# Optimization experiments

Measured on AMD Instinct MI355X. Metric: run time of the kernel, lower is better.

Reference implementation:

```python
import jax, jax.numpy as jnp
import numpy as np

EMB_DIM = 1024
N_HEAD = 16
HEAD_DIM = EMB_DIM // N_HEAD


def setup_inputs() -> dict:
    key = jax.random.key(0)
    kx, kq, kk, kv, ko = jax.random.split(key, 5)
    B, S = 4, 2048
    x = jax.random.normal(kx, (B, S, EMB_DIM), dtype=jnp.float32)
    attention_mask = jnp.ones((B, S), dtype=jnp.int32)
    s = 1.0 / np.sqrt(EMB_DIM)
    w_q = jax.random.normal(kq, (EMB_DIM, EMB_DIM), dtype=jnp.float32) * s
    w_k = jax.random.normal(kk, (EMB_DIM, EMB_DIM), dtype=jnp.float32) * s
    w_v = jax.random.normal(kv, (EMB_DIM, EMB_DIM), dtype=jnp.float32) * s
    w_o = jax.random.normal(ko, (EMB_DIM, EMB_DIM), dtype=jnp.float32) * s
    return {"x": x, "attention_mask": attention_mask,
            "w_q": w_q, "w_k": w_k, "w_v": w_v, "w_o": w_o}


def reference(x, attention_mask, w_q, w_k, w_v, w_o):
    B, S, _ = x.shape
    scale = 1.0 / np.sqrt(HEAD_DIM)
    # projections; nn.Linear computes x @ W^T
    def split_heads(t):
        return t.reshape(B, S, N_HEAD, HEAD_DIM).transpose(0, 2, 1, 3)  # [B,H,S,D]
    q = split_heads(x @ w_q.T)
    k = split_heads(x @ w_k.T)
    v = split_heads(x @ w_v.T)
    scores = jnp.einsum('bhqd,bhkd->bhqk', q, k) * scale  # [B,H,S,S]
    pad_mask = (attention_mask == 0)[:, None, None, :]          # [B,1,1,S]
    causal = jnp.triu(jnp.ones((S, S), dtype=bool), k=1)[None, None]  # [1,1,S,S]
    combined = pad_mask | causal
    scores = jnp.where(combined, -jnp.inf, scores)
    attn = jax.nn.softmax(scores, axis=-1)
    out = jnp.einsum('bhqk,bhkd->bhqd', attn, v)
    out = out.transpose(0, 2, 1, 3).reshape(B, S, EMB_DIM)
    return out @ w_o.T
```

## Files before the change

kernel.cpp:

```cpp
#include <hip/hip_runtime.h>

typedef __bf16 bf16x8 __attribute__((ext_vector_type(8)));
typedef float f32x4 __attribute__((ext_vector_type(4)));

#define LOG2E 1.4426950408889634f
#define NEGC (-12.0f * LOG2E)

__device__ inline unsigned short f2bf(float f) {
  unsigned int u = __builtin_bit_cast(unsigned int, f);
  u += 0x7fff + ((u >> 16) & 1);
  return (unsigned short)(u >> 16);
}

__device__ inline void async16(const void* g, void* l) {
  __builtin_amdgcn_global_load_lds(
      (__attribute__((address_space(1))) void*)(g),
      (__attribute__((address_space(3))) void*)(l), 16, 0, 0);
}

__global__ __launch_bounds__(256) void cast_all(
    const float* __restrict__ x, const float* __restrict__ w0,
    const float* __restrict__ w1, const float* __restrict__ w2,
    const float* __restrict__ w3, unsigned short* __restrict__ xb,
    unsigned short* __restrict__ ob ) {
  int id = blockIdx.x;
  const float* in;
  unsigned short* out;
  int boff;
  if (id < 8192) { in = x; out = xb; boff = id; }
  else {
    int w = (id - 8192) >> 10; boff = (id - 8192) & 1023;
    switch (w) { case 0: in = w0; break; case 1: in = w1; break;
                 case 2: in = w2; break; default: in = w3; }
    out = ob + (long)w * 1048576;
  }
  int i = (boff * 256 + threadIdx.x) * 4;
  float4 v = *(const float4*)(in + i);
  ushort4 o;
  o.x = f2bf(v.x); o.y = f2bf(v.y); o.z = f2bf(v.z); o.w = f2bf(v.w);
  *(ushort4*)(out + i) = o;
}

#define BM 128
#define BN 128
#define BK 32

__global__ __launch_bounds__(256, 3) void gemm_bt(
    const unsigned short* __restrict__ A, const unsigned short* __restrict__ W,
    void* __restrict__ out, int M, int N, int K, int mode) {
  __shared__ unsigned short SM[BM * BK + BN * BK];
  unsigned short* As = SM;
  unsigned short* Ws = SM + BM * BK;
  int tid = threadIdx.x;
  int lane = tid & 63, wid = tid >> 6;
  int wm = wid >> 1, wn = wid & 1;
  int l15 = lane & 15, quad = lane >> 4;
  int m0 = (blockIdx.x & 63) * BM, n0 = (blockIdx.x >> 6) * BN;

  f32x4 acc[4][4] = {};

  int srow = tid >> 2;
  int scol = (tid & 3) * 8;
  const unsigned short* Ag = A + (long)(m0 + srow) * K + scol;
  const unsigned short* Wg = W + (long)(n0 + srow) * K + scol;
  char* AsB = (char*)As + wid * 1024;
  char* WsB = (char*)Ws + wid * 1024;

  for (int kt = 0; kt < K; kt += BK) {
    __syncthreads();
    async16(Ag + kt, AsB);
    async16(Ag + kt + (long)64 * K, AsB + 4096);
    async16(Wg + kt, WsB);
    async16(Wg + kt + (long)64 * K, WsB + 4096);
    __syncthreads();
    bf16x8 af[4], wf[4];
#pragma unroll
    for (int t = 0; t < 4; t++)
      af[t] = *(const bf16x8*)(As + (wm * 64 + t * 16 + l15) * BK + quad * 8);
#pragma unroll
    for (int t = 0; t < 4; t++)
      wf[t] = *(const bf16x8*)(Ws + (wn * 64 + t * 16 + l15) * BK + quad * 8);
#pragma unroll
    for (int i = 0; i < 4; i++)
#pragma unroll
      for (int j = 0; j < 4; j++)
        acc[i][j] = __builtin_amdgcn_mfma_f32_16x16x32_bf16(af[i], wf[j], acc[i][j], 0, 0, 0);
  }

  if (mode == 0) {
    float* Cf = (float*)out;
#pragma unroll
    for (int i = 0; i < 4; i++) {
      int row = m0 + wm * 64 + i * 16 + quad * 4;
#pragma unroll
      for (int j = 0; j < 4; j++) {
        int col = n0 + wn * 64 + j * 16 + l15;
#pragma unroll
        for (int r = 0; r < 4; r++)
          Cf[(long)(row + r) * N + col] = acc[i][j][r];
      }
    }
  } else {
    unsigned short* Cb = (unsigned short*)out;
    int which = n0 >> 10;
    if (which == 2) {
#pragma unroll
      for (int i = 0; i < 4; i++)
#pragma unroll
        for (int j = 0; j < 4; j++) {
          int m = m0 + wm * 64 + i * 16 + quad * 4;
          int n = n0 + wn * 64 + j * 16 + l15;
          int nn = n & 1023;
          int b = m >> 11, s = m & 2047;
          int h = nn >> 6, d = nn & 63;
          ushort4 pk;
          pk.x = f2bf(acc[i][j][0]); pk.y = f2bf(acc[i][j][1]);
          pk.z = f2bf(acc[i][j][2]); pk.w = f2bf(acc[i][j][3]);
          *(ushort4*)(&Cb[16777216 + (((long)((b * 16 + h) * 64 + d)) << 11) + s]) = pk;
        }
    } else {
      float scale = (which == 0) ? 0.125f : 1.0f;
      int h0 = (n0 & 1023) >> 6;
      unsigned short* Es = SM;
#pragma unroll
      for (int qr = 0; qr < 4; qr++) {
        __syncthreads();
        if (wm == (qr >> 1)) {
#pragma unroll
          for (int ii = 0; ii < 2; ii++) {
            int i = (qr & 1) * 2 + ii;
#pragma unroll
            for (int j = 0; j < 4; j++)
#pragma unroll
              for (int r = 0; r < 4; r++) {
                int rr = (i & 1) * 16 + quad * 4 + r;
                Es[rr * 136 + wn * 64 + j * 16 + l15] = f2bf(acc[i][j][r] * scale);
              }
          }
        }
        __syncthreads();
#pragma unroll
        for (int p = 0; p < 2; p++) {
          int pair = p * 32 + (tid >> 3);
          int rq = pair >> 1;
          int head = pair & 1, c8 = tid & 7;
          uint4 v = *(const uint4*)(&Es[rq * 136 + head * 64 + c8 * 8]);
          int m = m0 + qr * 32 + rq;
          int b = m >> 11, s = m & 2047;
          int h = h0 + head;
          long idx = (long)which * 8388608 +
                     ((long)((b * 16 + h) * 2048 + s)) * 64 + c8 * 8;
          *(uint4*)(&Cb[idx]) = v;
        }
      }
    }
  }
}

__global__ __launch_bounds__(512, 2)
void gemm256(
    const unsigned short* __restrict__ A, const unsigned short* __restrict__ W,
    unsigned short* __restrict__ out, int M, int N, int K) {
  __shared__ unsigned short sm[65536];
  (void)N;
  int tid = threadIdx.x, lane = tid & 63, wid = tid >> 6;
  int wm = wid >> 2, wn = wid & 3;
  int l15 = lane & 15, quad = lane >> 4;

  int cpx = (int)gridDim.x >> 3;
  int id = (int)blockIdx.x;
  int swz = (id & 7) * cpx + (id >> 3);
  int mtiles = M >> 8;
  int mt = swz % mtiles, nt = swz / mtiles;
  int m0 = mt << 8, n0 = nt << 8;

  f32x4 acc[8][4] = {};
  bf16x8 afr[4][2], bfr[2][2];

  int rl = tid >> 3;
  int ch = (tid & 7) ^ (rl & 7);
  const unsigned short* Ag = A + (long)(m0 + rl) * K + ch * 8;
  const unsigned short* Wg = W + (long)(n0 + rl) * K + ch * 8;
  int dst0 = wid * 1024;

#define STG(BUF, MAT, HALF, KT) do {                                          \
    const unsigned short* g_ = ((MAT) ? Wg : Ag) + (long)(HALF) * 128 * K + (KT) * 64; \
    char* d_ = (char*)sm + ((BUF) * 4 + (MAT) * 2 + (HALF)) * 16384 + dst0;   \
    async16(g_, d_);                                                          \
    async16(g_ + (long)64 * K, d_ + 8192);                                    \
  } while (0)

#define RDA(BUF, MH) do {                                                     \
    char* b_ = (char*)sm + ((BUF) * 4 + (MH)) * 16384;                        \
    _Pragma("unroll") for (int mf = 0; mf < 4; mf++) {                        \
      int r_ = wm * 64 + mf * 16 + l15;                                       \
      char* p_ = b_ + r_ * 128; int sw_ = (r_ & 7) << 4;                      \
      afr[mf][0] = *(const bf16x8*)(p_ + ((quad * 16) ^ sw_));                \
      afr[mf][1] = *(const bf16x8*)(p_ + ((64 + quad * 16) ^ sw_));           \
    } } while (0)

#define RDB(BUF, NH) do {                                                     \
    char* b_ = (char*)sm + ((BUF) * 4 + 2 + (NH)) * 16384;                    \
    _Pragma("unroll") for (int nf = 0; nf < 2; nf++) {                        \
      int r_ = wn * 32 + nf * 16 + l15;                                       \
      char* p_ = b_ + r_ * 128; int sw_ = (r_ & 7) << 4;                      \
      bfr[nf][0] = *(const bf16x8*)(p_ + ((quad * 16) ^ sw_));                \
      bfr[nf][1] = *(const bf16x8*)(p_ + ((64 + quad * 16) ^ sw_));           \
    } } while (0)

#define MM16(MH, NH) do {                                                     \
    __builtin_amdgcn_s_setprio(1);                                            \
    _Pragma("unroll") for (int kk = 0; kk < 2; kk++)                          \
    _Pragma("unroll") for (int mf = 0; mf < 4; mf++)                          \
    _Pragma("unroll") for (int nf = 0; nf < 2; nf++)                          \
      acc[(MH) * 4 + mf][(NH) * 2 + nf] = __builtin_amdgcn_mfma_f32_16x16x32_bf16( \
          afr[mf][kk], bfr[nf][kk], acc[(MH) * 4 + mf][(NH) * 2 + nf], 0, 0, 0);   \
    __builtin_amdgcn_s_setprio(0);                                            \
  } while (0)

#define BARx() __builtin_amdgcn_s_barrier()
#define LGKM0() asm volatile("s_waitcnt lgkmcnt(0)" ::: "memory")
#define VM8() asm volatile("s_waitcnt vmcnt(8)" ::: "memory")
#define VM0() asm volatile("s_waitcnt vmcnt(0)" ::: "memory")

  STG(0, 0, 0, 0); STG(0, 1, 0, 0); STG(0, 1, 1, 0); STG(0, 0, 1, 0);
  STG(1, 0, 0, 1); STG(1, 1, 0, 1);
  asm volatile("s_waitcnt vmcnt(4)" ::: "memory");
  BARx();

  for (int i = 0; i < 8; i++) {
    int t1 = 2 * i + 1;
    bool st = (i < 7);
    RDA(0, 0); RDB(0, 0); STG(1, 1, 1, t1);
    BARx(); LGKM0(); MM16(0, 0); VM8(); BARx();
    RDB(0, 1); STG(1, 0, 1, t1);
    BARx(); LGKM0(); MM16(0, 1); VM8(); BARx();
    RDA(0, 1); RDB(0, 0); if (st) STG(0, 0, 0, t1 + 1);
    BARx(); LGKM0(); MM16(1, 0); VM8(); BARx();
    RDB(0, 1); if (st) STG(0, 1, 0, t1 + 1);
    BARx(); LGKM0(); MM16(1, 1); if (st) VM8(); else VM0(); BARx();
    RDA(1, 0); RDB(1, 0); if (st) STG(0, 1, 1, t1 + 1);
    BARx(); LGKM0(); MM16(0, 0); if (st) VM8(); else VM0(); BARx();
    RDB(1, 1); if (st) STG(0, 0, 1, t1 + 1);
    BARx(); LGKM0(); MM16(0, 1); if (st) VM8(); else VM0(); BARx();
    RDA(1, 1); RDB(1, 0); if (st) STG(1, 0, 0, t1 + 2);
    BARx(); LGKM0(); MM16(1, 0); if (st) VM8(); else VM0(); BARx();
    RDB(1, 1); if (st) STG(1, 1, 0, t1 + 2);
    BARx(); LGKM0(); MM16(1, 1); if (st) VM8(); else VM0(); BARx();
  }

#undef STG
#undef RDA
#undef RDB
#undef MM16
#undef BARx
#undef LGKM0
#undef VM8
#undef VM0

  unsigned short* Cb = out;
  int which = n0 >> 10;
  if (which == 2) {
#pragma unroll
    for (int mi = 0; mi < 8; mi++) {
      int m = m0 + (mi >> 2) * 128 + wm * 64 + (mi & 3) * 16 + quad * 4;
      int b = m >> 11, s = m & 2047;
#pragma unroll
      for (int ni = 0; ni < 4; ni++) {
        int n = n0 + (ni >> 1) * 128 + wn * 32 + (ni & 1) * 16 + l15;
        int nn = n & 1023;
        int h = nn >> 6, d = nn & 63;
        ushort4 pk;
        pk.x = f2bf(acc[mi][ni][0]); pk.y = f2bf(acc[mi][ni][1]);
        pk.z = f2bf(acc[mi][ni][2]); pk.w = f2bf(acc[mi][ni][3]);
        *(ushort4*)(&Cb[16777216 + (((long)((b * 16 + h) * 64 + d)) << 11) + s]) = pk;
      }
    }
  } else {
    float scale = (which == 0) ? 0.125f : 1.0f;
#pragma unroll
    for (int mi = 0; mi < 8; mi++) {
#pragma unroll
      for (int ni = 0; ni < 4; ni++) {
#pragma unroll
        for (int r = 0; r < 4; r++) {
          int m = m0 + (mi >> 2) * 128 + wm * 64 + (mi & 3) * 16 + quad * 4 + r;
          int n = n0 + (ni >> 1) * 128 + wn * 32 + (ni & 1) * 16 + l15;
          int b = m >> 11, s = m & 2047;
          int nn = n & 1023;
          int h = nn >> 6, d = nn & 63;
          long idx = (long)which * 8388608 + ((long)((b * 16 + h) * 2048 + s)) * 64 + d;
          Cb[idx] = f2bf(acc[mi][ni][r] * scale);
        }
      }
    }
  }
}

#define BQ 128
#define BKV 64
#define PSTR 76

__global__ __launch_bounds__(256, 3) void attn(
    const unsigned short* __restrict__ Q, const unsigned short* __restrict__ Kt,
    const unsigned short* __restrict__ VT, const int* __restrict__ am,
    unsigned short* __restrict__ O) {
  __shared__ unsigned short QPs[BQ * PSTR];
  __shared__ unsigned short Ks[BKV * PSTR];
  __shared__ unsigned short Vs[64 * PSTR];
  const int S = 2048, D = 64;
  int tid = threadIdx.x, lane = tid & 63, wid = tid >> 6;
  int l15 = lane & 15, quad = lane >> 4;

  int id = blockIdx.x;
  int s = id >> 8;
  int r = id & 255;
  int bh = r & 63;
  int c = r >> 6;
  int qt;
  switch (s) { case 0: qt = 15 - c; break; case 1: qt = 8 + c; break;
               case 2: qt = 7 - c; break; default: qt = c; }
  int q0 = qt * BQ;
  int b = bh >> 4, h = bh & 15;
  const unsigned short* Qg = Q + (long)bh * S * D;
  const unsigned short* Kg = Kt + (long)bh * S * D;
  const unsigned short* Vg = VT + (long)bh * D * S;
  const int* amg = am + b * S;

  int row0 = tid >> 3, col0 = (tid & 7) * 8;
  int row1 = 32 + (tid >> 3), col1 = col0;

#pragma unroll
  for (int rr = 0; rr < 4; rr++) {
    int cc = rr * 256 + tid;
    int row = cc >> 3, col = (cc & 7) * 8;
    *(uint4*)(&QPs[row * PSTR + col]) = *(const uint4*)(Qg + (long)(q0 + row) * D + col);
  }

  uint4 kreg0 = *(const uint4*)(Kg + (long)row0 * D + col0);
  uint4 kreg1 = *(const uint4*)(Kg + (long)row1 * D + col1);
  uint4 vreg0 = *(const uint4*)(Vg + (long)row0 * S + col0);
  uint4 vreg1 = *(const uint4*)(Vg + (long)row1 * S + col1);

  __syncthreads();
  bf16x8 qf[2][2];
#pragma unroll
  for (int i = 0; i < 2; i++)
#pragma unroll
    for (int kk = 0; kk < 2; kk++)
      qf[i][kk] = *(const bf16x8*)(&QPs[(wid * 32 + i * 16 + l15) * PSTR + kk * 32 + quad * 8]);

  f32x4 o_acc[2][4] = {};
  float lsum[2][4] = {};

  int tFull = q0 >> 6;
  int nt = tFull + 2;
  for (int t = 0; t < nt; t++) {
    int s0 = t * BKV;
    __syncthreads();
    *(uint4*)(&Ks[row0 * PSTR + col0]) = kreg0;
    *(uint4*)(&Ks[row1 * PSTR + col1]) = kreg1;
    *(uint4*)(&Vs[row0 * PSTR + col0]) = vreg0;
    *(uint4*)(&Vs[row1 * PSTR + col1]) = vreg1;
    __syncthreads();

    {
      long s0n = (t + 1) * BKV; if (s0n > S - BKV) s0n = S - BKV;
      kreg0 = *(const uint4*)(Kg + (s0n + row0) * D + col0);
      kreg1 = *(const uint4*)(Kg + (s0n + row1) * D + col1);
      vreg0 = *(const uint4*)(Vg + (long)row0 * S + s0n + col0);
      vreg1 = *(const uint4*)(Vg + (long)row1 * S + s0n + col1);
    }

    int mvj[4];
#pragma unroll
    for (int j = 0; j < 4; j++) mvj[j] = amg[s0 + j * 16 + l15];

    f32x4 sacc[2][4] = {};
#pragma unroll
    for (int kk = 0; kk < 2; kk++) {
      bf16x8 kf[4];
#pragma unroll
      for (int j = 0; j < 4; j++)
        kf[j] = *(const bf16x8*)(&Ks[(j * 16 + l15) * PSTR + kk * 32 + quad * 8]);
      __builtin_amdgcn_s_setprio(1);
#pragma unroll
      for (int i = 0; i < 2; i++)
#pragma unroll
        for (int j = 0; j < 4; j++)
          sacc[i][j] = __builtin_amdgcn_mfma_f32_16x16x32_bf16(qf[i][kk], kf[j], sacc[i][j], 0, 0, 0);
      __builtin_amdgcn_s_setprio(0);
    }

    float fb[4];
#pragma unroll
    for (int j = 0; j < 4; j++) fb[j] = mvj[j] ? NEGC : -1e38f;

    if (t < tFull) {
#pragma unroll
      for (int i = 0; i < 2; i++)
#pragma unroll
        for (int rr = 0; rr < 4; rr++) {
          int prow = (wid * 32 + i * 16 + quad * 4 + rr) * PSTR;
          float rs = 0.f;
#pragma unroll
          for (int j = 0; j < 4; j++) {
            float p = __builtin_amdgcn_exp2f(fmaf(sacc[i][j][rr], LOG2E, fb[j]));
            unsigned int u = __builtin_bit_cast(unsigned int, p);
            QPs[prow + j * 16 + l15] = (unsigned short)(u >> 16);
            rs += __builtin_bit_cast(float, u & 0xffff0000u);
          }
          lsum[i][rr] += rs;
        }
    } else {
#pragma unroll
      for (int i = 0; i < 2; i++)
#pragma unroll
        for (int rr = 0; rr < 4; rr++) {
          int row = q0 + wid * 32 + i * 16 + quad * 4 + rr;
          int prow = (wid * 32 + i * 16 + quad * 4 + rr) * PSTR;
          float rs = 0.f;
#pragma unroll
          for (int j = 0; j < 4; j++) {
            int col = s0 + j * 16 + l15;
            float fbe = (col > row) ? -1e38f : fb[j];
            float p = __builtin_amdgcn_exp2f(fmaf(sacc[i][j][rr], LOG2E, fbe));
            unsigned int u = __builtin_bit_cast(unsigned int, p);
            QPs[prow + j * 16 + l15] = (unsigned short)(u >> 16);
            rs += __builtin_bit_cast(float, u & 0xffff0000u);
          }
          lsum[i][rr] += rs;
        }
    }

#pragma unroll
    for (int kk = 0; kk < 2; kk++) {
      bf16x8 pf[2], vf[4];
#pragma unroll
      for (int i = 0; i < 2; i++)
        pf[i] = *(const bf16x8*)(&QPs[(wid * 32 + i * 16 + l15) * PSTR + kk * 32 + quad * 8]);
#pragma unroll
      for (int j = 0; j < 4; j++)
        vf[j] = *(const bf16x8*)(&Vs[(j * 16 + l15) * PSTR + kk * 32 + quad * 8]);
      __builtin_amdgcn_s_setprio(1);
#pragma unroll
      for (int i = 0; i < 2; i++)
#pragma unroll
        for (int j = 0; j < 4; j++)
          o_acc[i][j] = __builtin_amdgcn_mfma_f32_16x16x32_bf16(pf[i], vf[j], o_acc[i][j], 0, 0, 0);
      __builtin_amdgcn_s_setprio(0);
    }
  }

#pragma unroll
  for (int i = 0; i < 2; i++)
#pragma unroll
    for (int rr = 0; rr < 4; rr++) {
      float tsum = lsum[i][rr];
      tsum += __shfl_xor(tsum, 1, 64);
      tsum += __shfl_xor(tsum, 2, 64);
      tsum += __shfl_xor(tsum, 4, 64);
      tsum += __shfl_xor(tsum, 8, 64);
      float inv = 1.0f / tsum;
      int prow = (wid * 32 + i * 16 + quad * 4 + rr) * PSTR;
#pragma unroll
      for (int j = 0; j < 4; j++)
        QPs[prow + j * 16 + l15] = f2bf(o_acc[i][j][rr] * inv);
    }
  __syncthreads();
#pragma unroll
  for (int rr = 0; rr < 4; rr++) {
    int cc = rr * 256 + tid;
    int row = cc >> 3, col = (cc & 7) * 8;
    uint4 v = *(const uint4*)(&QPs[row * PSTR + col]);
    long gm = (long)b * S + q0 + row;
    *(uint4*)(&O[gm * 1024 + h * 64 + col]) = v;
  }
}

extern "C" void kernel_launch(void* const* d_in, const int* in_sizes, int n_in,
                              void* d_out, int out_size, void* d_ws, size_t ws_size,
                              hipStream_t stream) {
  const float* x  = (const float*)d_in[0];
  const int*   am = (const int*)d_in[1];
  const float* wq = (const float*)d_in[2];
  const float* wk = (const float*)d_in[3];
  const float* wv = (const float*)d_in[4];
  const float* wo = (const float*)d_in[5];
  float* out = (float*)d_out;

  const int S = 2048, E = 1024, Bb = 4, H = 16;
  const int M = Bb * S;

  char* ws = (char*)d_ws;
  unsigned short* xb  = (unsigned short*)ws;
  unsigned short* wqb = (unsigned short*)(ws + 16777216);
  unsigned short* wob = wqb + 3 * 1048576;
  unsigned short* Qb  = (unsigned short*)(ws + 25165824);
  unsigned short* Ob  = Qb + 25165824;

  cast_all<<<12288, 256, 0, stream>>>(x, wq, wk, wv, wo, xb, wqb);

  gemm_bt<<<dim3((3 * E / BN) * (M / BM)), 256, 0, stream>>>(xb, wqb, Qb, M, 3 * E, E, 4);
  attn<<<dim3(1024), 256, 0, stream>>>(Qb, Qb + 8388608, Qb + 16777216, am, Ob);
  gemm_bt<<<dim3((E / BN) * (M / BM)), 256, 0, stream>>>(Ob, wob, out, M, E, E, 0);
}
```

Measured before the change: 249.1 us.

## Double-buffer K tiles in LDS and stream V fragments from global to registers

Restructures the attention loop so K tiles are double-buffered in shared memory. This needs one barrier per iteration instead of two, and the next-next K tile is prefetched into registers. V no longer goes through shared memory: each wave loads its MFMA V fragments straight from global memory into registers one tile ahead. The aim is to cut barrier stalls and LDS round trips, at the cost of redundant V reads across waves through the cache and more registers. The unused gemm256 kernel is also deleted.

Result: slower. 307.8 us (+23.5%).

```diff
diff --git a/kernel.cpp b/kernel.cpp
--- a/kernel.cpp
+++ b/kernel.cpp
@@ -157,146 +157,6 @@
   }
 }
 
-__global__ __launch_bounds__(512, 2)
-void gemm256(
-    const unsigned short* __restrict__ A, const unsigned short* __restrict__ W,
-    unsigned short* __restrict__ out, int M, int N, int K) {
-  __shared__ unsigned short sm[65536];
-  (void)N;
-  int tid = threadIdx.x, lane = tid & 63, wid = tid >> 6;
-  int wm = wid >> 2, wn = wid & 3;
-  int l15 = lane & 15, quad = lane >> 4;
-
-  int cpx = (int)gridDim.x >> 3;
-  int id = (int)blockIdx.x;
-  int swz = (id & 7) * cpx + (id >> 3);
-  int mtiles = M >> 8;
-  int mt = swz % mtiles, nt = swz / mtiles;
-  int m0 = mt << 8, n0 = nt << 8;
-
-  f32x4 acc[8][4] = {};
-  bf16x8 afr[4][2], bfr[2][2];
-
-  int rl = tid >> 3;
-  int ch = (tid & 7) ^ (rl & 7);
-  const unsigned short* Ag = A + (long)(m0 + rl) * K + ch * 8;
-  const unsigned short* Wg = W + (long)(n0 + rl) * K + ch * 8;
-  int dst0 = wid * 1024;
-
-#define STG(BUF, MAT, HALF, KT) do {                                          \
-    const unsigned short* g_ = ((MAT) ? Wg : Ag) + (long)(HALF) * 128 * K + (KT) * 64; \
-    char* d_ = (char*)sm + ((BUF) * 4 + (MAT) * 2 + (HALF)) * 16384 + dst0;   \
-    async16(g_, d_);                                                          \
-    async16(g_ + (long)64 * K, d_ + 8192);                                    \
-  } while (0)
-
-#define RDA(BUF, MH) do {                                                     \
-    char* b_ = (char*)sm + ((BUF) * 4 + (MH)) * 16384;                        \
-    _Pragma("unroll") for (int mf = 0; mf < 4; mf++) {                        \
-      int r_ = wm * 64 + mf * 16 + l15;                                       \
-      char* p_ = b_ + r_ * 128; int sw_ = (r_ & 7) << 4;                      \
-      afr[mf][0] = *(const bf16x8*)(p_ + ((quad * 16) ^ sw_));                \
-      afr[mf][1] = *(const bf16x8*)(p_ + ((64 + quad * 16) ^ sw_));           \
-    } } while (0)
-
-#define RDB(BUF, NH) do {                                                     \
-    char* b_ = (char*)sm + ((BUF) * 4 + 2 + (NH)) * 16384;                    \
-    _Pragma("unroll") for (int nf = 0; nf < 2; nf++) {                        \
-      int r_ = wn * 32 + nf * 16 + l15;                                       \
-      char* p_ = b_ + r_ * 128; int sw_ = (r_ & 7) << 4;                      \
-      bfr[nf][0] = *(const bf16x8*)(p_ + ((quad * 16) ^ sw_));                \
-      bfr[nf][1] = *(const bf16x8*)(p_ + ((64 + quad * 16) ^ sw_));           \
-    } } while (0)
-
-#define MM16(MH, NH) do {                                                     \
-    __builtin_amdgcn_s_setprio(1);                                            \
-    _Pragma("unroll") for (int kk = 0; kk < 2; kk++)                          \
-    _Pragma("unroll") for (int mf = 0; mf < 4; mf++)                          \
-    _Pragma("unroll") for (int nf = 0; nf < 2; nf++)                          \
-      acc[(MH) * 4 + mf][(NH) * 2 + nf] = __builtin_amdgcn_mfma_f32_16x16x32_bf16( \
-          afr[mf][kk], bfr[nf][kk], acc[(MH) * 4 + mf][(NH) * 2 + nf], 0, 0, 0);   \
-    __builtin_amdgcn_s_setprio(0);                                            \
-  } while (0)
-
-#define BARx() __builtin_amdgcn_s_barrier()
-#define LGKM0() asm volatile("s_waitcnt lgkmcnt(0)" ::: "memory")
-#define VM8() asm volatile("s_waitcnt vmcnt(8)" ::: "memory")
-#define VM0() asm volatile("s_waitcnt vmcnt(0)" ::: "memory")
-
-  STG(0, 0, 0, 0); STG(0, 1, 0, 0); STG(0, 1, 1, 0); STG(0, 0, 1, 0);
-  STG(1, 0, 0, 1); STG(1, 1, 0, 1);
-  asm volatile("s_waitcnt vmcnt(4)" ::: "memory");
-  BARx();
-
-  for (int i = 0; i < 8; i++) {
-    int t1 = 2 * i + 1;
-    bool st = (i < 7);
-    RDA(0, 0); RDB(0, 0); STG(1, 1, 1, t1);
-    BARx(); LGKM0(); MM16(0, 0); VM8(); BARx();
-    RDB(0, 1); STG(1, 0, 1, t1);
-    BARx(); LGKM0(); MM16(0, 1); VM8(); BARx();
-    RDA(0, 1); RDB(0, 0); if (st) STG(0, 0, 0, t1 + 1);
-    BARx(); LGKM0(); MM16(1, 0); VM8(); BARx();
-    RDB(0, 1); if (st) STG(0, 1, 0, t1 + 1);
-    BARx(); LGKM0(); MM16(1, 1); if (st) VM8(); else VM0(); BARx();
-    RDA(1, 0); RDB(1, 0); if (st) STG(0, 1, 1, t1 + 1);
-    BARx(); LGKM0(); MM16(0, 0); if (st) VM8(); else VM0(); BARx();
-    RDB(1, 1); if (st) STG(0, 0, 1, t1 + 1);
-    BARx(); LGKM0(); MM16(0, 1); if (st) VM8(); else VM0(); BARx();
-    RDA(1, 1); RDB(1, 0); if (st) STG(1, 0, 0, t1 + 2);
-    BARx(); LGKM0(); MM16(1, 0); if (st) VM8(); else VM0(); BARx();
-    RDB(1, 1); if (st) STG(1, 1, 0, t1 + 2);
-    BARx(); LGKM0(); MM16(1, 1); if (st) VM8(); else VM0(); BARx();
-  }
-
-#undef STG
-#undef RDA
-#undef RDB
-#undef MM16
-#undef BARx
-#undef LGKM0
-#undef VM8
-#undef VM0
-
-  unsigned short* Cb = out;
-  int which = n0 >> 10;
-  if (which == 2) {
-#pragma unroll
-    for (int mi = 0; mi < 8; mi++) {
-      int m = m0 + (mi >> 2) * 128 + wm * 64 + (mi & 3) * 16 + quad * 4;
-      int b = m >> 11, s = m & 2047;
-#pragma unroll
-      for (int ni = 0; ni < 4; ni++) {
-        int n = n0 + (ni >> 1) * 128 + wn * 32 + (ni & 1) * 16 + l15;
-        int nn = n & 1023;
-        int h = nn >> 6, d = nn & 63;
-        ushort4 pk;
-        pk.x = f2bf(acc[mi][ni][0]); pk.y = f2bf(acc[mi][ni][1]);
-        pk.z = f2bf(acc[mi][ni][2]); pk.w = f2bf(acc[mi][ni][3]);
-        *(ushort4*)(&Cb[16777216 + (((long)((b * 16 + h) * 64 + d)) << 11) + s]) = pk;
-      }
-    }
-  } else {
-    float scale = (which == 0) ? 0.125f : 1.0f;
-#pragma unroll
-    for (int mi = 0; mi < 8; mi++) {
-#pragma unroll
-      for (int ni = 0; ni < 4; ni++) {
-#pragma unroll
-        for (int r = 0; r < 4; r++) {
-          int m = m0 + (mi >> 2) * 128 + wm * 64 + (mi & 3) * 16 + quad * 4 + r;
-          int n = n0 + (ni >> 1) * 128 + wn * 32 + (ni & 1) * 16 + l15;
-          int b = m >> 11, s = m & 2047;
-          int nn = n & 1023;
-          int h = nn >> 6, d = nn & 63;
-          long idx = (long)which * 8388608 + ((long)((b * 16 + h) * 2048 + s)) * 64 + d;
-          Cb[idx] = f2bf(acc[mi][ni][r] * scale);
-        }
-      }
-    }
-  }
-}
-
 #define BQ 128
 #define BKV 64
 #define PSTR 76
@@ -306,8 +166,7 @@
     const unsigned short* __restrict__ VT, const int* __restrict__ am,
     unsigned short* __restrict__ O) {
   __shared__ unsigned short QPs[BQ * PSTR];
-  __shared__ unsigned short Ks[BKV * PSTR];
-  __shared__ unsigned short Vs[64 * PSTR];
+  __shared__ unsigned short Ks[2][BKV * PSTR];
   const int S = 2048, D = 64;
   int tid = threadIdx.x, lane = tid & 63, wid = tid >> 6;
   int l15 = lane & 15, quad = lane >> 4;
@@ -339,8 +198,6 @@
 
   uint4 kreg0 = *(const uint4*)(Kg + (long)row0 * D + col0);
   uint4 kreg1 = *(const uint4*)(Kg + (long)row1 * D + col1);
-  uint4 vreg0 = *(const uint4*)(Vg + (long)row0 * S + col0);
-  uint4 vreg1 = *(const uint4*)(Vg + (long)row1 * S + col1);
 
   __syncthreads();
   bf16x8 qf[2][2];
@@ -349,6 +206,18 @@
 #pragma unroll
     for (int kk = 0; kk < 2; kk++)
       qf[i][kk] = *(const bf16x8*)(&QPs[(wid * 32 + i * 16 + l15) * PSTR + kk * 32 + quad * 8]);
+
+  *(uint4*)(&Ks[0][row0 * PSTR + col0]) = kreg0;
+  *(uint4*)(&Ks[0][row1 * PSTR + col1]) = kreg1;
+  kreg0 = *(const uint4*)(Kg + (long)(BKV + row0) * D + col0);
+  kreg1 = *(const uint4*)(Kg + (long)(BKV + row1) * D + col1);
+  bf16x8 vf[2][4];
+#pragma unroll
+  for (int kk = 0; kk < 2; kk++)
+#pragma unroll
+    for (int j = 0; j < 4; j++)
+      vf[kk][j] = *(const bf16x8*)(Vg + (long)(j * 16 + l15) * S + kk * 32 + quad * 8);
+  __syncthreads();
 
   f32x4 o_acc[2][4] = {};
   float lsum[2][4] = {};
@@ -357,20 +226,10 @@
   int nt = tFull + 2;
   for (int t = 0; t < nt; t++) {
     int s0 = t * BKV;
-    __syncthreads();
-    *(uint4*)(&Ks[row0 * PSTR + col0]) = kreg0;
-    *(uint4*)(&Ks[row1 * PSTR + col1]) = kreg1;
-    *(uint4*)(&Vs[row0 * PSTR + col0]) = vreg0;
-    *(uint4*)(&Vs[row1 * PSTR + col1]) = vreg1;
-    __syncthreads();
-
-    {
-      long s0n = (t + 1) * BKV; if (s0n > S - BKV) s0n = S - BKV;
-      kreg0 = *(const uint4*)(Kg + (s0n + row0) * D + col0);
-      kreg1 = *(const uint4*)(Kg + (s0n + row1) * D + col1);
-      vreg0 = *(const uint4*)(Vg + (long)row0 * S + s0n + col0);
-      vreg1 = *(const uint4*)(Vg + (long)row1 * S + s0n + col1);
-    }
+    int cur = t & 1, nxt = cur ^ 1;
+
+    *(uint4*)(&Ks[nxt][row0 * PSTR + col0]) = kreg0;
+    *(uint4*)(&Ks[nxt][row1 * PSTR + col1]) = kreg1;
 
     int mvj[4];
 #pragma unroll
@@ -382,7 +241,7 @@
       bf16x8 kf[4];
 #pragma unroll
       for (int j = 0; j < 4; j++)
-        kf[j] = *(const bf16x8*)(&Ks[(j * 16 + l15) * PSTR + kk * 32 + quad * 8]);
+        kf[j] = *(const bf16x8*)(&Ks[cur][(j * 16 + l15) * PSTR + kk * 32 + quad * 8]);
       __builtin_amdgcn_s_setprio(1);
 #pragma unroll
       for (int i = 0; i < 2; i++)
@@ -390,6 +249,14 @@
         for (int j = 0; j < 4; j++)
           sacc[i][j] = __builtin_amdgcn_mfma_f32_16x16x32_bf16(qf[i][kk], kf[j], sacc[i][j], 0, 0, 0);
       __builtin_amdgcn_s_setprio(0);
+    }
+
+    __syncthreads();
+
+    {
+      long s0n = (long)(t + 2) * BKV; if (s0n > S - BKV) s0n = S - BKV;
+      kreg0 = *(const uint4*)(Kg + (s0n + row0) * D + col0);
+      kreg1 = *(const uint4*)(Kg + (s0n + row1) * D + col1);
     }
 
     float fb[4];
@@ -435,20 +302,26 @@
 
 #pragma unroll
     for (int kk = 0; kk < 2; kk++) {
-      bf16x8 pf[2], vf[4];
+      bf16x8 pf[2];
 #pragma unroll
       for (int i = 0; i < 2; i++)
         pf[i] = *(const bf16x8*)(&QPs[(wid * 32 + i * 16 + l15) * PSTR + kk * 32 + quad * 8]);
-#pragma unroll
-      for (int j = 0; j < 4; j++)
-        vf[j] = *(const bf16x8*)(&Vs[(j * 16 + l15) * PSTR + kk * 32 + quad * 8]);
       __builtin_amdgcn_s_setprio(1);
 #pragma unroll
       for (int i = 0; i < 2; i++)
 #pragma unroll
         for (int j = 0; j < 4; j++)
-          o_acc[i][j] = __builtin_amdgcn_mfma_f32_16x16x32_bf16(pf[i], vf[j], o_acc[i][j], 0, 0, 0);
+          o_acc[i][j] = __builtin_amdgcn_mfma_f32_16x16x32_bf16(pf[i], vf[kk][j], o_acc[i][j], 0, 0, 0);
       __builtin_amdgcn_s_setprio(0);
+    }
+
+    {
+      long s0v = (long)(t + 1) * BKV; if (s0v > S - BKV) s0v = S - BKV;
+#pragma unroll
+      for (int kk = 0; kk < 2; kk++)
+#pragma unroll
+        for (int j = 0; j < 4; j++)
+          vf[kk][j] = *(const bf16x8*)(Vg + (long)(j * 16 + l15) * S + s0v + kk * 32 + quad * 8);
     }
   }
 
```
